# Kernel tuning notes

Measured on AMD Instinct MI355X. Metric: run time of the kernel, lower is better.

The kernel has to match this reference:

```python
import jax, jax.numpy as jnp
import numpy as np

B, S, D = 2, 1024, 4096
NQ, NKV, HD = 32, 8, 128
G = NQ // NKV
FFN = 10928  # ffn_size(4096, 4.0): int(4*4096)*2//3 = 10922 -> round up to mult of 8
ATTN_MULT = 0.08838834764831845
MAX_ATTN = 30.0
EPS = 1e-5
BASE = 10000.0


def setup_inputs() -> dict:
    key = jax.random.key(0)
    ks = jax.random.split(key, 13)
    def w(k, shape):
        return jax.random.normal(k, shape, jnp.float32) / np.float32(np.sqrt(shape[0]))
    return {
        "x": jax.random.normal(ks[0], (B, S, D), jnp.float32),
        "mask": jnp.tril(jnp.ones((1, 1, S, S), dtype=bool)),  # causal
        "scale_pre_attn": jax.random.uniform(ks[1], (D,), jnp.float32, 0.5, 1.5),
        "scale_post_attn": jax.random.uniform(ks[2], (D,), jnp.float32, 0.5, 1.5),
        "scale_pre_mlp": jax.random.uniform(ks[3], (D,), jnp.float32, 0.5, 1.5),
        "scale_post_mlp": jax.random.uniform(ks[4], (D,), jnp.float32, 0.5, 1.5),
        "wq": w(ks[5], (D, NQ * HD)),
        "wk": w(ks[6], (D, NKV * HD)),
        "wv": w(ks[7], (D, NKV * HD)),
        "wo": w(ks[8], (NQ * HD, D)),
        "w_gate": w(ks[9], (D, FFN)),
        "w_val": w(ks[10], (D, FFN)),
        "w_out": w(ks[11], (FFN, D)),
    }


def rms_norm(x, scale):
    ms = jnp.mean(jnp.square(x), axis=-1, keepdims=True)
    return x * jax.lax.rsqrt(ms + EPS) * scale


def rotate_half(x):
    x1, x2 = jnp.split(x, 2, axis=-1)
    return jnp.concatenate((-x2, x1), axis=-1)


def apply_rope(x):
    # x: [b, s, h, d]; offset=0 (no KV-cache step)
    s, d = x.shape[1], x.shape[3]
    inv_freq = 1.0 / (BASE ** (jnp.arange(0, d, 2, dtype=jnp.float32) / d))
    t = jnp.arange(s, dtype=jnp.float32)
    phase = t[:, None] * inv_freq[None, :]            # [s, d/2]
    phase = jnp.tile(phase, (1, 2))[None, :, None, :]  # [1, s, 1, d]
    return (x * jnp.cos(phase) + rotate_half(x) * jnp.sin(phase)).astype(x.dtype)


def reference(x, mask, scale_pre_attn, scale_post_attn, scale_pre_mlp, scale_post_mlp,
              wq, wk, wv, wo, w_gate, w_val, w_out):
    h = x
    # ---- attention sublayer (pre-norm) ----
    hn = rms_norm(h, scale_pre_attn)
    q = (hn @ wq).reshape(B, S, NQ, HD)
    k = (hn @ wk).reshape(B, S, NKV, HD)
    v = (hn @ wv).reshape(B, S, NKV, HD)
    q = apply_rope(q)
    k = apply_rope(k)
    qg = q.reshape(B, S, NKV, G, HD)  # GQA: group q heads per kv head
    logits = jnp.einsum("btkgd,bskd->bkgts", qg, k).astype(jnp.float32) * ATTN_MULT
    logits = MAX_ATTN * jnp.tanh(logits / MAX_ATTN)   # grok soft cap
    logits = jnp.where(mask[:, :, None], logits, -1e30)
    probs = jax.nn.softmax(logits, axis=-1).astype(x.dtype)
    attn = jnp.einsum("bkgts,bskd->btkgd", probs, v).reshape(B, S, NQ * HD)
    h_attn = attn @ wo
    h = h + rms_norm(h_attn, scale_post_attn)
    # ---- gated MLP sublayer (pre-norm) ----
    hn2 = rms_norm(h, scale_pre_mlp)
    h_dense = (jax.nn.gelu(hn2 @ w_gate) * (hn2 @ w_val)) @ w_out
    h = h + rms_norm(h_dense, scale_post_mlp)
    return h
```

## Files before the change

### kernel.cpp

```cpp
#include <hip/hip_runtime.h>
#include <stdint.h>

typedef unsigned short ushort_t;
typedef __bf16 bf16x8 __attribute__((ext_vector_type(8)));
typedef float f32x4 __attribute__((ext_vector_type(4)));

#define D_MODEL 4096
#define SEQ 1024
#define BROWS 2048
#define QKV_N 6144
#define HD 128
#define FFN_PAD 10944
#define FFN_GRID 11008
#define ATTN_MULT 0.08838834764831845f

__device__ __forceinline__ unsigned short f2bf(float f){
  union { float f; unsigned u; } c; c.f = f;
  unsigned u = c.u + 0x7fffu + ((c.u >> 16) & 1u);
  return (unsigned short)(u >> 16);
}
__device__ __forceinline__ float bf2f(unsigned short h){
  union { unsigned u; float f; } c; c.u = ((unsigned)h) << 16;
  return c.f;
}
__device__ __forceinline__ f32x4 zero4(){ f32x4 z; z[0]=0.f; z[1]=0.f; z[2]=0.f; z[3]=0.f; return z; }
__device__ __forceinline__ bf16x8 ldb8(const void* p){ return *(const bf16x8*)p; }
__device__ __forceinline__ f32x4 MFMA(bf16x8 a, bf16x8 b, f32x4 c){
  return __builtin_amdgcn_mfma_f32_16x16x32_bf16(a, b, c, 0, 0, 0);
}
__device__ __forceinline__ void g2lds16(void* lds, const void* g){
  __builtin_amdgcn_global_load_lds(
      (const __attribute__((address_space(1))) void*)(uintptr_t)(g),
      (__attribute__((address_space(3))) void*)(uint32_t)(uintptr_t)(lds),
      16, 0, 0);
}
#define BAR() __builtin_amdgcn_s_barrier()
#define VMCNT6() asm volatile("s_waitcnt vmcnt(6)" ::: "memory")
#define VMCNT0() asm volatile("s_waitcnt vmcnt(0)" ::: "memory")

__global__ __launch_bounds__(256) void rmsnorm_in(const float* __restrict__ x,
                                                  const float* __restrict__ sc,
                                                  ushort_t* __restrict__ out){
  int row = blockIdx.x, tid = threadIdx.x;
  const float4* xr = (const float4*)(x + (size_t)row*D_MODEL);
  float4 v[4]; float ss = 0.f;
#pragma unroll
  for (int i=0;i<4;i++){
    v[i] = xr[tid + i*256];
    ss += v[i].x*v[i].x + v[i].y*v[i].y + v[i].z*v[i].z + v[i].w*v[i].w;
  }
#pragma unroll
  for (int m=32;m;m>>=1) ss += __shfl_xor(ss, m);
  __shared__ float red[4];
  if ((tid&63)==0) red[tid>>6] = ss;
  __syncthreads();
  float inv = rsqrtf((red[0]+red[1]+red[2]+red[3])*(1.f/4096.f) + 1e-5f);
  const float4* scv = (const float4*)sc;
#pragma unroll
  for (int i=0;i<4;i++){
    float4 s4 = scv[tid + i*256];
    ushort4 o;
    o.x = f2bf(v[i].x*inv*s4.x); o.y = f2bf(v[i].y*inv*s4.y);
    o.z = f2bf(v[i].z*inv*s4.z); o.w = f2bf(v[i].w*inv*s4.w);
    ((ushort4*)out)[(size_t)row*1024 + tid + i*256] = o;
  }
}

__global__ __launch_bounds__(256) void rmsnorm_resid(const float* __restrict__ base,
                                                     const float* __restrict__ delta,
                                                     const float* __restrict__ sc1,
                                                     float* __restrict__ hout,
                                                     const float* __restrict__ sc2,
                                                     ushort_t* __restrict__ hn2){
  int row = blockIdx.x, tid = threadIdx.x;
  const float4* dr = (const float4*)(delta + (size_t)row*D_MODEL);
  const float4* br = (const float4*)(base  + (size_t)row*D_MODEL);
  float4 d[4]; float ss = 0.f;
#pragma unroll
  for (int i=0;i<4;i++){
    d[i] = dr[tid + i*256];
    ss += d[i].x*d[i].x + d[i].y*d[i].y + d[i].z*d[i].z + d[i].w*d[i].w;
  }
#pragma unroll
  for (int m=32;m;m>>=1) ss += __shfl_xor(ss, m);
  __shared__ float red[4];
  if ((tid&63)==0) red[tid>>6] = ss;
  __syncthreads();
  float inv1 = rsqrtf((red[0]+red[1]+red[2]+red[3])*(1.f/4096.f) + 1e-5f);
  const float4* s1v = (const float4*)sc1;
  float4* ho = (float4*)(hout + (size_t)row*D_MODEL);
  float4 h4[4]; float ss2 = 0.f;
#pragma unroll
  for (int i=0;i<4;i++){
    float4 b4 = br[tid + i*256];
    float4 s4 = s1v[tid + i*256];
    float4 h;
    h.x = b4.x + d[i].x*inv1*s4.x;
    h.y = b4.y + d[i].y*inv1*s4.y;
    h.z = b4.z + d[i].z*inv1*s4.z;
    h.w = b4.w + d[i].w*inv1*s4.w;
    h4[i] = h;
    ho[tid + i*256] = h;
    ss2 += h.x*h.x + h.y*h.y + h.z*h.z + h.w*h.w;
  }
  if (sc2){
#pragma unroll
    for (int m=32;m;m>>=1) ss2 += __shfl_xor(ss2, m);
    __syncthreads();
    if ((tid&63)==0) red[tid>>6] = ss2;
    __syncthreads();
    float inv2 = rsqrtf((red[0]+red[1]+red[2]+red[3])*(1.f/4096.f) + 1e-5f);
    const float4* s2v = (const float4*)sc2;
#pragma unroll
    for (int i=0;i<4;i++){
      float4 s4 = s2v[tid + i*256];
      ushort4 o;
      o.x = f2bf(h4[i].x*inv2*s4.x); o.y = f2bf(h4[i].y*inv2*s4.y);
      o.z = f2bf(h4[i].z*inv2*s4.z); o.w = f2bf(h4[i].w*inv2*s4.w);
      ((ushort4*)hn2)[(size_t)row*1024 + tid + i*256] = o;
    }
  }
}

__global__ __launch_bounds__(256) void convT(const float* __restrict__ W,
                                             ushort_t* __restrict__ WT,
                                             int K, int N, int Kp, int Np){
  __shared__ float tile[64][33];
  int n0 = blockIdx.x*32, k0 = blockIdx.y*64;
  int tx = threadIdx.x & 31, ty = threadIdx.x >> 5;
#pragma unroll
  for (int i=0;i<8;i++){
    int k = k0 + ty + i*8, n = n0 + tx;
    tile[ty+i*8][tx] = (k < K && n < N) ? W[(size_t)k*N + n] : 0.f;
  }
  __syncthreads();
#pragma unroll
  for (int i=0;i<4;i++){
    int n = n0 + ty + i*8;
    if (n < Np){
      ushort2 o;
      o.x = f2bf(tile[tx*2  ][ty+i*8]);
      o.y = f2bf(tile[tx*2+1][ty+i*8]);
      *(ushort2*)&WT[(size_t)n*Kp + k0 + tx*2] = o;
    }
  }
}

template<int MODE>
__global__ __launch_bounds__(512, 2) void gemm256(const ushort_t* __restrict__ A, int lda,
                                                  const ushort_t* __restrict__ WT, int ldw,
                                                  void* __restrict__ Cv, int ldc,
                                                  int Nvalid, int K){
  __shared__ __align__(16) char smem[147456];
  const int nwg = gridDim.x;
  const int lid = blockIdx.x;
  const int t  = (lid & 7) * (nwg >> 3) + (lid >> 3);
  const int m0 = (t & 7) << 8;
  const int n0 = (t >> 3) << 7;
  const int tid = threadIdx.x;
  const int w = tid >> 6, lane = tid & 63;
  const int wm = w >> 1, wn = w & 1;
  const int lo = lane & 15, hi = lane >> 4;
  const int srow = lane >> 3, scol = lane & 7;
  const int sw = scol ^ srow;
  const int rsw = lo & 7;
  const int NT = K >> 6;

  const ushort_t* pA = A  + (size_t)(m0 + w*8 + srow) * lda + sw*8;
  const ushort_t* pB = WT + (size_t)(n0 + w*8 + srow) * ldw + sw*8;

  auto stage = [&](int tt, int slot, int c){
    const ushort_t* g = (c < 4 ? pA + (size_t)(c*64)*lda : pB + (size_t)((c-4)*64)*ldw) + tt*64;
    char* l = smem + slot*49152 + (c < 4 ? c*8192 : 32768 + (c-4)*8192) + (w<<10);
    g2lds16(l, g);
  };

  f32x4 acc[4][4];
#pragma unroll
  for (int i=0;i<4;i++)
#pragma unroll
    for (int j=0;j<4;j++) acc[i][j] = zero4();

#pragma unroll
  for (int c=0;c<6;c++) stage(0, 0, c);
#pragma unroll
  for (int c=0;c<6;c++) stage(1, 1, c);

  int cur = 0;
  for (int i=0;i<NT;i++){
    if (i == NT-1) VMCNT0(); else VMCNT6();
    BAR();
    const char* sA = smem + cur*49152;
    const char* sB = sA + 32768;
    const int nxt = (cur == 2) ? 0 : cur + 1;
    const int nn  = (nxt == 2) ? 0 : nxt + 1;
    if (i+2 < NT){
      stage(i+2, nn, 0); stage(i+2, nn, 1); stage(i+2, nn, 2);
      stage(i+2, nn, 3); stage(i+2, nn, 4); stage(i+2, nn, 5);
    }
    bf16x8 af[4][2], bfr[4][2];
#pragma unroll
    for (int rf=0;rf<4;rf++)
#pragma unroll
      for (int kc=0;kc<2;kc++)
        af[rf][kc] = ldb8(sA + (wm*64 + rf*16 + lo)*128 + (((kc*4+hi)^rsw)<<4));
#pragma unroll
    for (int cf=0;cf<4;cf++)
#pragma unroll
      for (int kc=0;kc<2;kc++)
        bfr[cf][kc] = ldb8(sB + (wn*64 + cf*16 + lo)*128 + (((kc*4+hi)^rsw)<<4));
#pragma unroll
    for (int rf=0;rf<4;rf++)
#pragma unroll
      for (int cf=0;cf<4;cf++)
#pragma unroll
        for (int kc=0;kc<2;kc++)
          acc[rf][cf] = MFMA(af[rf][kc], bfr[cf][kc], acc[rf][cf]);
    cur = nxt;
  }
#pragma unroll
  for (int rf=0;rf<4;rf++){
#pragma unroll
    for (int cf=0;cf<4;cf++){
#pragma unroll
      for (int r=0;r<4;r++){
        int m = m0 + wm*64 + rf*16 + hi*4 + r;
        int n = n0 + wn*64 + cf*16 + lo;
        if (n < Nvalid){
          float v = acc[rf][cf][r];
          size_t idx = (size_t)m*ldc + n;
          if (MODE == 1){
            ((float*)Cv)[idx] = v;
          } else if (MODE == 0){
            ((ushort_t*)Cv)[idx] = f2bf(v);
          } else {
            float g = bf2f(((ushort_t*)Cv)[idx]);
            float ga = 0.5f*g*(1.f + tanhf(0.7978845608028654f*(g + 0.044715f*g*g*g)));
            ((ushort_t*)Cv)[idx] = f2bf(ga * v);
          }
        }
      }
    }
  }
}

__global__ void rope_tab_kernel(float* __restrict__ tab){
  int s = blockIdx.x, i = threadIdx.x;
  float invf = __expf(-(float)i * (9.210340371976184f/64.f));
  float ph = (float)s * invf;
  float sn, cs;
  sincosf(ph, &sn, &cs);
  tab[s*128 + i] = cs;
  tab[s*128 + 64 + i] = sn;
}

__global__ __launch_bounds__(256) void rope_apply(ushort_t* __restrict__ qkv,
                                                  const float* __restrict__ tab){
  int idx = blockIdx.x*256 + threadIdx.x;
  int pr = idx & 63;
  int h  = (idx >> 6) % 40;
  int row = idx / 2560;
  int t = row & (SEQ-1);
  ushort_t* p = qkv + (size_t)row*QKV_N + h*HD + pr;
  float c = tab[t*128 + pr], s = tab[t*128 + 64 + pr];
  float x1 = bf2f(p[0]), x2 = bf2f(p[64]);
  p[0]  = f2bf(x1*c - x2*s);
  p[64] = f2bf(x2*c + x1*s);
}

__global__ __launch_bounds__(256) void transpose_v(const ushort_t* __restrict__ qkv,
                                                   ushort_t* __restrict__ VT){
  __shared__ ushort_t tile[32][33];
  int d0 = blockIdx.x*32, m0 = blockIdx.y*32;
  int tx = threadIdx.x & 31, ty = threadIdx.x >> 5;
#pragma unroll
  for (int i=0;i<4;i++)
    tile[ty + i*8][tx] = qkv[(size_t)(m0 + ty + i*8)*QKV_N + 5120 + d0 + tx];
  __syncthreads();
#pragma unroll
  for (int i=0;i<4;i++)
    VT[(size_t)(d0 + ty + i*8)*BROWS + m0 + tx] = tile[tx][ty + i*8];
}

__global__ __launch_bounds__(256) void attn_kernel(const ushort_t* __restrict__ qkv,
                                                   const ushort_t* __restrict__ VT,
                                                   ushort_t* __restrict__ outp){
  const int blk = blockIdx.x;
  const int bh = blk & 63;
  const int tgrp = 15 - (blk >> 6);
  const int b = bh >> 5, qh = bh & 31, kv = qh >> 2;
  const int w = threadIdx.x >> 6, lane = threadIdx.x & 63;
  const int lo = lane & 15, hi = lane >> 4;
  const int t0 = tgrp*64 + w*16;
  __shared__ ushort_t P[4][16][72];
  ushort_t (*Pw)[72] = P[w];

  const ushort_t* Qb = qkv + (size_t)(b*SEQ + t0 + lo)*QKV_N + qh*HD + hi*8;
  bf16x8 qf[4];
#pragma unroll
  for (int c=0;c<4;c++) qf[c] = ldb8(Qb + c*32);

  f32x4 of[8];
#pragma unroll
  for (int i=0;i<8;i++) of[i] = zero4();
  float ls[4] = {0.f,0.f,0.f,0.f};

  const ushort_t* Kb = qkv + (size_t)(b*SEQ + lo)*QKV_N + D_MODEL + kv*HD + hi*8;
  const ushort_t* Vb = VT + (size_t)(kv*HD + lo)*BROWS + b*SEQ + hi*8;

  const int nst = tgrp + 1;
  for (int st=0; st<nst; st++){
    const int s0 = st*64;
    f32x4 sacc[4];
#pragma unroll
    for (int nf=0;nf<4;nf++) sacc[nf] = zero4();
#pragma unroll
    for (int c=0;c<4;c++){
#pragma unroll
      for (int nf=0;nf<4;nf++){
        bf16x8 kf = ldb8(Kb + (size_t)(s0 + nf*16)*QKV_N + c*32);
        sacc[nf] = MFMA(qf[c], kf, sacc[nf]);
      }
    }
#pragma unroll
    for (int nf=0;nf<4;nf++){
#pragma unroll
      for (int r=0;r<4;r++){
        int tq = t0 + hi*4 + r;
        int s = s0 + nf*16 + lo;
        float xx = sacc[nf][r] * ATTN_MULT;
        float z = fminf(fmaxf(xx*(2.f/30.f), -80.f), 80.f);
        float e = __expf(z);
        float th = (e - 1.f)/(e + 1.f);
        float p = (s <= tq) ? __expf(30.f*th - 30.f) : 0.f;
        ls[r] += p;
        Pw[hi*4+r][nf*16+lo] = f2bf(p);
      }
    }
    __builtin_amdgcn_sched_barrier(0);
    __builtin_amdgcn_s_waitcnt(0xc07f);
    __builtin_amdgcn_sched_barrier(0);
#pragma unroll
    for (int c2=0;c2<2;c2++){
      bf16x8 pf = ldb8(&Pw[lo][c2*32 + hi*8]);
#pragma unroll
      for (int nf2=0;nf2<8;nf2++){
        bf16x8 vf = ldb8(Vb + (size_t)(nf2*16)*BROWS + s0 + c2*32);
        of[nf2] = MFMA(pf, vf, of[nf2]);
      }
    }
    __builtin_amdgcn_sched_barrier(0);
  }
#pragma unroll
  for (int m=1;m<16;m<<=1){
#pragma unroll
    for (int r=0;r<4;r++) ls[r] += __shfl_xor(ls[r], m);
  }
  float inv[4];
#pragma unroll
  for (int r=0;r<4;r++) inv[r] = 1.f/ls[r];
  ushort_t* Ob = outp + (size_t)(b*SEQ + t0 + hi*4)*D_MODEL + qh*HD + lo;
#pragma unroll
  for (int nf2=0;nf2<8;nf2++)
#pragma unroll
    for (int r=0;r<4;r++)
      Ob[(size_t)r*D_MODEL + nf2*16] = f2bf(of[nf2][r]*inv[r]);
}

extern "C" void kernel_launch(void* const* d_in, const int* in_sizes, int n_in,
                              void* d_out, int out_size, void* d_ws, size_t ws_size,
                              hipStream_t stream){
  const float* x        = (const float*)d_in[0];
  const float* sc_pre_a = (const float*)d_in[2];
  const float* sc_post_a= (const float*)d_in[3];
  const float* sc_pre_m = (const float*)d_in[4];
  const float* sc_post_m= (const float*)d_in[5];
  const float* wq  = (const float*)d_in[6];
  const float* wk  = (const float*)d_in[7];
  const float* wv  = (const float*)d_in[8];
  const float* wo  = (const float*)d_in[9];
  const float* wg  = (const float*)d_in[10];
  const float* wva = (const float*)d_in[11];
  const float* wou = (const float*)d_in[12];

  char* ws = (char*)d_ws;
  size_t off = 0;
  auto alloc = [&](size_t bytes)->void*{
    void* p = ws + off; off += (bytes + 255) & ~(size_t)255; return p;
  };
  ushort_t* WT   = (ushort_t*)alloc((size_t)FFN_GRID*D_MODEL*2);
  ushort_t* hn   = (ushort_t*)alloc((size_t)BROWS*D_MODEL*2);
  ushort_t* qkv  = (ushort_t*)alloc((size_t)BROWS*QKV_N*2);
  ushort_t* VT   = (ushort_t*)alloc((size_t)SEQ*BROWS*2);
  ushort_t* attn = (ushort_t*)alloc((size_t)BROWS*D_MODEL*2);
  float*    tmp32= (float*)alloc((size_t)BROWS*D_MODEL*4);
  ushort_t* hn2  = (ushort_t*)alloc((size_t)BROWS*D_MODEL*2);
  ushort_t* act  = (ushort_t*)alloc((size_t)BROWS*FFN_PAD*2);
  float*    rtab = (float*)alloc((size_t)SEQ*128*4);
  float* h = (float*)d_out;

  rmsnorm_in<<<BROWS, 256, 0, stream>>>(x, sc_pre_a, hn);
  convT<<<dim3(4096/32, 4096/64), 256, 0, stream>>>(wq, WT,                     4096, 4096, 4096, 4096);
  convT<<<dim3(1024/32, 4096/64), 256, 0, stream>>>(wk, WT + (size_t)4096*4096, 4096, 1024, 4096, 1024);
  convT<<<dim3(1024/32, 4096/64), 256, 0, stream>>>(wv, WT + (size_t)5120*4096, 4096, 1024, 4096, 1024);
  gemm256<0><<<384, 512, 0, stream>>>(hn, 4096, WT, 4096, qkv, QKV_N, QKV_N, 4096);
  rope_tab_kernel<<<SEQ, 64, 0, stream>>>(rtab);
  rope_apply<<<(BROWS*40*64)/256, 256, 0, stream>>>(qkv, rtab);
  transpose_v<<<dim3(32,64), 256, 0, stream>>>(qkv, VT);
  attn_kernel<<<1024, 256, 0, stream>>>(qkv, VT, attn);
  convT<<<dim3(4096/32, 4096/64), 256, 0, stream>>>(wo, WT, 4096, 4096, 4096, 4096);
  gemm256<1><<<256, 512, 0, stream>>>(attn, 4096, WT, 4096, tmp32, 4096, 4096, 4096);
  rmsnorm_resid<<<BROWS, 256, 0, stream>>>(x, tmp32, sc_post_a, h, sc_pre_m, hn2);
  convT<<<dim3(FFN_GRID/32, 4096/64), 256, 0, stream>>>(wg, WT, 4096, 10928, 4096, FFN_GRID);
  gemm256<0><<<688, 512, 0, stream>>>(hn2, 4096, WT, 4096, act, FFN_PAD, FFN_PAD, 4096);
  convT<<<dim3(FFN_GRID/32, 4096/64), 256, 0, stream>>>(wva, WT, 4096, 10928, 4096, FFN_GRID);
  gemm256<2><<<688, 512, 0, stream>>>(hn2, 4096, WT, 4096, act, FFN_PAD, FFN_PAD, 4096);
  convT<<<dim3(4096/32, FFN_PAD/64), 256, 0, stream>>>(wou, WT, 10928, 4096, FFN_PAD, 4096);
  gemm256<1><<<256, 512, 0, stream>>>(act, FFN_PAD, WT, FFN_PAD, tmp32, 4096, 4096, FFN_PAD);
  rmsnorm_resid<<<BROWS, 256, 0, stream>>>(h, tmp32, sc_post_m, h, nullptr, nullptr);
}
```

Before: 1.282 ms.

## Fuse gate and value FFN GEMMs into one kernel and widen weight transpose tiles

Adds a dual-B GEMM kernel that computes the gate and value projections together. Each A tile of hn2 is loaded once and multiplied against both transposed weights, with GELU times value applied in the epilogue. This removes the second full GEMM pass and the read-modify-write of the act buffer. The gate/value transposes now go to separate buffers, the second one aliasing the no-longer-needed hn/qkv workspace region. The convT transpose also moves to 64x64 tiles with ushort4 stores to cut launch count and use wider writes. The price is double the accumulator registers per thread in the fused kernel, which raises spill risk.

```diff
diff --git a/kernel.cpp b/kernel.cpp
--- a/kernel.cpp
+++ b/kernel.cpp
@@ -36,7 +36,9 @@
 }
 #define BAR() __builtin_amdgcn_s_barrier()
 #define VMCNT6() asm volatile("s_waitcnt vmcnt(6)" ::: "memory")
+#define VMCNT8() asm volatile("s_waitcnt vmcnt(8)" ::: "memory")
 #define VMCNT0() asm volatile("s_waitcnt vmcnt(0)" ::: "memory")
+#define LGKM0() asm volatile("s_waitcnt lgkmcnt(0)" ::: "memory")
 
 __global__ __launch_bounds__(256) void rmsnorm_in(const float* __restrict__ x,
                                                   const float* __restrict__ sc,
@@ -125,23 +127,26 @@
 __global__ __launch_bounds__(256) void convT(const float* __restrict__ W,
                                              ushort_t* __restrict__ WT,
                                              int K, int N, int Kp, int Np){
-  __shared__ float tile[64][33];
-  int n0 = blockIdx.x*32, k0 = blockIdx.y*64;
-  int tx = threadIdx.x & 31, ty = threadIdx.x >> 5;
-#pragma unroll
-  for (int i=0;i<8;i++){
-    int k = k0 + ty + i*8, n = n0 + tx;
-    tile[ty+i*8][tx] = (k < K && n < N) ? W[(size_t)k*N + n] : 0.f;
+  __shared__ float tile[64][65];
+  int n0 = blockIdx.x*64, k0 = blockIdx.y*64;
+  int tx = threadIdx.x & 63, ty = threadIdx.x >> 6;
+#pragma unroll
+  for (int i=0;i<16;i++){
+    int k = k0 + ty + i*4, n = n0 + tx;
+    tile[ty+i*4][tx] = (k < K && n < N) ? W[(size_t)k*N + n] : 0.f;
   }
   __syncthreads();
-#pragma unroll
-  for (int i=0;i<4;i++){
-    int n = n0 + ty + i*8;
+  int wtx = threadIdx.x & 15, wty = threadIdx.x >> 4;
+#pragma unroll
+  for (int j=0;j<4;j++){
+    int n = n0 + wty + j*16;
     if (n < Np){
-      ushort2 o;
-      o.x = f2bf(tile[tx*2  ][ty+i*8]);
-      o.y = f2bf(tile[tx*2+1][ty+i*8]);
-      *(ushort2*)&WT[(size_t)n*Kp + k0 + tx*2] = o;
+      ushort4 o;
+      o.x = f2bf(tile[wtx*4+0][wty + j*16]);
+      o.y = f2bf(tile[wtx*4+1][wty + j*16]);
+      o.z = f2bf(tile[wtx*4+2][wty + j*16]);
+      o.w = f2bf(tile[wtx*4+3][wty + j*16]);
+      *(ushort4*)&WT[(size_t)n*Kp + k0 + wtx*4] = o;
     }
   }
 }
@@ -170,7 +175,7 @@
   const ushort_t* pB = WT + (size_t)(n0 + w*8 + srow) * ldw + sw*8;
 
   auto stage = [&](int tt, int slot, int c){
-    const ushort_t* g = (c < 4 ? pA + (size_t)(c*64)*lda : pB + (size_t)((c-4)*64)*ldw) + tt*64;
+    const ushort_t* g = (c < 4 ? pA + (size_t)(c*64)*lda : pB + (size_t)((c-4)*64)*ldw) + (size_t)tt*64;
     char* l = smem + slot*49152 + (c < 4 ? c*8192 : 32768 + (c-4)*8192) + (w<<10);
     g2lds16(l, g);
   };
@@ -229,15 +234,106 @@
         if (n < Nvalid){
           float v = acc[rf][cf][r];
           size_t idx = (size_t)m*ldc + n;
-          if (MODE == 1){
-            ((float*)Cv)[idx] = v;
-          } else if (MODE == 0){
-            ((ushort_t*)Cv)[idx] = f2bf(v);
-          } else {
-            float g = bf2f(((ushort_t*)Cv)[idx]);
-            float ga = 0.5f*g*(1.f + tanhf(0.7978845608028654f*(g + 0.044715f*g*g*g)));
-            ((ushort_t*)Cv)[idx] = f2bf(ga * v);
-          }
+          if (MODE == 1) ((float*)Cv)[idx] = v;
+          else           ((ushort_t*)Cv)[idx] = f2bf(v);
+        }
+      }
+    }
+  }
+}
+
+__global__ __launch_bounds__(512, 2) void gemm_gv(const ushort_t* __restrict__ A, int lda,
+                                                  const ushort_t* __restrict__ B1,
+                                                  const ushort_t* __restrict__ B2, int ldw,
+                                                  ushort_t* __restrict__ Cv, int ldc,
+                                                  int Nvalid, int K){
+  __shared__ __align__(16) char smem[131072];
+  const int nwg = gridDim.x;
+  const int lid = blockIdx.x;
+  const int t  = (lid & 7) * (nwg >> 3) + (lid >> 3);
+  const int m0 = (t & 7) << 8;
+  const int n0 = (t >> 3) << 7;
+  const int tid = threadIdx.x;
+  const int w = tid >> 6, lane = tid & 63;
+  const int wm = w >> 1, wn = w & 1;
+  const int lo = lane & 15, hi = lane >> 4;
+  const int srow = lane >> 3, scol = lane & 7;
+  const int sw = scol ^ srow;
+  const int rsw = lo & 7;
+  const int NT = K >> 6;
+
+  const ushort_t* pA  = A  + (size_t)(m0 + w*8 + srow) * lda + sw*8;
+  const ushort_t* pB1 = B1 + (size_t)(n0 + w*8 + srow) * ldw + sw*8;
+  const ushort_t* pB2 = B2 + (size_t)(n0 + w*8 + srow) * ldw + sw*8;
+
+  auto stage = [&](int tt, int c){
+    const ushort_t* g;
+    int lofs;
+    if (c < 4){ g = pA  + (size_t)(c*64)*lda;     lofs = c*8192; }
+    else if (c < 6){ g = pB1 + (size_t)((c-4)*64)*ldw; lofs = 32768 + (c-4)*8192; }
+    else { g = pB2 + (size_t)((c-6)*64)*ldw; lofs = 49152 + (c-6)*8192; }
+    g2lds16(smem + ((tt&1)<<16) + lofs + (w<<10), g + (size_t)tt*64);
+  };
+
+  f32x4 ag[4][4], av[4][4];
+#pragma unroll
+  for (int i=0;i<4;i++)
+#pragma unroll
+    for (int j=0;j<4;j++){ ag[i][j] = zero4(); av[i][j] = zero4(); }
+
+#pragma unroll
+  for (int c=0;c<8;c++) stage(0, c);
+#pragma unroll
+  for (int c=0;c<8;c++) stage(1, c);
+
+  for (int i=0;i<NT;i++){
+    if (i == NT-1) VMCNT0(); else VMCNT8();
+    BAR();
+    const char* sA  = smem + ((i&1)<<16);
+    const char* sB1 = sA + 32768;
+    const char* sB2 = sA + 49152;
+    bf16x8 af[4][2], b1f[4][2], b2f[4][2];
+#pragma unroll
+    for (int rf=0;rf<4;rf++)
+#pragma unroll
+      for (int kc=0;kc<2;kc++)
+        af[rf][kc] = ldb8(sA + (wm*64 + rf*16 + lo)*128 + (((kc*4+hi)^rsw)<<4));
+#pragma unroll
+    for (int cf=0;cf<4;cf++)
+#pragma unroll
+      for (int kc=0;kc<2;kc++){
+        b1f[cf][kc] = ldb8(sB1 + (wn*64 + cf*16 + lo)*128 + (((kc*4+hi)^rsw)<<4));
+        b2f[cf][kc] = ldb8(sB2 + (wn*64 + cf*16 + lo)*128 + (((kc*4+hi)^rsw)<<4));
+      }
+    LGKM0();
+    BAR();
+    if (i+2 < NT){
+#pragma unroll
+      for (int c=0;c<8;c++) stage(i+2, c);
+    }
+#pragma unroll
+    for (int rf=0;rf<4;rf++)
+#pragma unroll
+      for (int cf=0;cf<4;cf++)
+#pragma unroll
+        for (int kc=0;kc<2;kc++){
+          ag[rf][cf] = MFMA(af[rf][kc], b1f[cf][kc], ag[rf][cf]);
+          av[rf][cf] = MFMA(af[rf][kc], b2f[cf][kc], av[rf][cf]);
+        }
+  }
+#pragma unroll
+  for (int rf=0;rf<4;rf++){
+#pragma unroll
+    for (int cf=0;cf<4;cf++){
+#pragma unroll
+      for (int r=0;r<4;r++){
+        int m = m0 + wm*64 + rf*16 + hi*4 + r;
+        int n = n0 + wn*64 + cf*16 + lo;
+        if (n < Nvalid){
+          float g = ag[rf][cf][r];
+          float v = av[rf][cf][r];
+          float ga = 0.5f*g*(1.f + tanhf(0.7978845608028654f*(g + 0.044715f*g*g*g)));
+          Cv[(size_t)m*ldc + n] = f2bf(ga * v);
         }
       }
     }
@@ -398,24 +494,24 @@
   ushort_t* act  = (ushort_t*)alloc((size_t)BROWS*FFN_PAD*2);
   float*    rtab = (float*)alloc((size_t)SEQ*128*4);
   float* h = (float*)d_out;
+  ushort_t* WT2  = (ushort_t*)hn;
 
   rmsnorm_in<<<BROWS, 256, 0, stream>>>(x, sc_pre_a, hn);
-  convT<<<dim3(4096/32, 4096/64), 256, 0, stream>>>(wq, WT,                     4096, 4096, 4096, 4096);
-  convT<<<dim3(1024/32, 4096/64), 256, 0, stream>>>(wk, WT + (size_t)4096*4096, 4096, 1024, 4096, 1024);
-  convT<<<dim3(1024/32, 4096/64), 256, 0, stream>>>(wv, WT + (size_t)5120*4096, 4096, 1024, 4096, 1024);
+  convT<<<dim3(64, 64), 256, 0, stream>>>(wq, WT,                     4096, 4096, 4096, 4096);
+  convT<<<dim3(16, 64), 256, 0, stream>>>(wk, WT + (size_t)4096*4096, 4096, 1024, 4096, 1024);
+  convT<<<dim3(16, 64), 256, 0, stream>>>(wv, WT + (size_t)5120*4096, 4096, 1024, 4096, 1024);
   gemm256<0><<<384, 512, 0, stream>>>(hn, 4096, WT, 4096, qkv, QKV_N, QKV_N, 4096);
   rope_tab_kernel<<<SEQ, 64, 0, stream>>>(rtab);
   rope_apply<<<(BROWS*40*64)/256, 256, 0, stream>>>(qkv, rtab);
   transpose_v<<<dim3(32,64), 256, 0, stream>>>(qkv, VT);
   attn_kernel<<<1024, 256, 0, stream>>>(qkv, VT, attn);
-  convT<<<dim3(4096/32, 4096/64), 256, 0, stream>>>(wo, WT, 4096, 4096, 4096, 4096);
+  convT<<<dim3(64, 64), 256, 0, stream>>>(wo, WT, 4096, 4096, 4096, 4096);
   gemm256<1><<<256, 512, 0, stream>>>(attn, 4096, WT, 4096, tmp32, 4096, 4096, 4096);
   rmsnorm_resid<<<BROWS, 256, 0, stream>>>(x, tmp32, sc_post_a, h, sc_pre_m, hn2);
-  convT<<<dim3(FFN_GRID/32, 4096/64), 256, 0, stream>>>(wg, WT, 4096, 10928, 4096, FFN_GRID);
-  gemm256<0><<<688, 512, 0, stream>>>(hn2, 4096, WT, 4096, act, FFN_PAD, FFN_PAD, 4096);
-  convT<<<dim3(FFN_GRID/32, 4096/64), 256, 0, stream>>>(wva, WT, 4096, 10928, 4096, FFN_GRID);
-  gemm256<2><<<688, 512, 0, stream>>>(hn2, 4096, WT, 4096, act, FFN_PAD, FFN_PAD, 4096);
-  convT<<<dim3(4096/32, FFN_PAD/64), 256, 0, stream>>>(wou, WT, 10928, 4096, FFN_PAD, 4096);
+  convT<<<dim3(172, 64), 256, 0, stream>>>(wg,  WT,  4096, 10928, 4096, FFN_GRID);
+  convT<<<dim3(172, 64), 256, 0, stream>>>(wva, WT2, 4096, 10928, 4096, FFN_GRID);
+  gemm_gv<<<688, 512, 0, stream>>>(hn2, 4096, WT, WT2, 4096, act, FFN_PAD, FFN_PAD, 4096);
+  convT<<<dim3(64, 171), 256, 0, stream>>>(wou, WT, 10928, 4096, FFN_PAD, 4096);
   gemm256<1><<<256, 512, 0, stream>>>(act, FFN_PAD, WT, FFN_PAD, tmp32, 4096, 4096, FFN_PAD);
   rmsnorm_resid<<<BROWS, 256, 0, stream>>>(h, tmp32, sc_post_m, h, nullptr, nullptr);
 }
```

Measured after the change: 1.211 ms. 5.5% less time.
